# Performance work log

Measured on AMD Instinct MI355X. Metric: run time of the kernel, lower is better.

Reference implementation:

```python
import jax, jax.numpy as jnp
import numpy as np

D_MODEL = 1024
N_EXPERTS = 16
D_FF = 4 * D_MODEL
B, T = 2, 2048


def setup_inputs() -> dict:
    key = jax.random.key(0)
    ks = jax.random.split(key, 6)
    s1 = 1.0 / np.sqrt(D_MODEL)
    s2 = 1.0 / np.sqrt(D_FF)
    return {
        "x": jax.random.normal(ks[0], (B, T, D_MODEL), dtype=jnp.float32),
        "W1": jax.random.normal(ks[1], (N_EXPERTS, D_MODEL, D_FF), dtype=jnp.float32) * s1,
        "b1": jnp.zeros((N_EXPERTS, D_FF), dtype=jnp.float32),
        "W2": jax.random.normal(ks[2], (N_EXPERTS, D_FF, D_MODEL), dtype=jnp.float32) * s2,
        "b2": jnp.zeros((N_EXPERTS, D_MODEL), dtype=jnp.float32),
        "Wg": jax.random.normal(ks[3], (D_MODEL, N_EXPERTS), dtype=jnp.float32) * s1,
        "k": 2,
    }


def reference(x, W1, b1, W2, b2, Wg, k):
    # Gating: [B,T,E] logits, top-k, softmax over selected logits
    gate_logits = jnp.einsum("btd,de->bte", x, Wg)
    topk_vals, topk_idx = jax.lax.top_k(gate_logits, k)      # [B,T,k]
    weights = jax.nn.softmax(topk_vals, axis=-1)             # [B,T,k]
    # Dense all-expert FFN (faithful to the original which computes every expert)
    h = jax.nn.swish(jnp.einsum("btd,edf->btef", x, W1) + b1)        # [B,T,E,4D]
    expert_out = jnp.einsum("btef,efd->bted", h, W2) + b2            # [B,T,E,D]
    # Gather top-k expert outputs per token and combine
    sel = jnp.take_along_axis(expert_out, topk_idx[..., None], axis=2)  # [B,T,k,D]
    return jnp.sum(sel * weights[..., None], axis=2)                    # [B,T,D]
```

## Files before the change

### kernel.cpp

```cpp
#include <hip/hip_runtime.h>
#include <cstdint>

#define D_MODEL 1024
#define N_EXP   16
#define D_FF    4096
#define NTOK    4096
#define NSEL    8192

typedef uint16_t u16;
typedef __bf16    bf16x8 __attribute__((ext_vector_type(8)));
typedef uint16_t  u16x8  __attribute__((ext_vector_type(8)));
typedef float     f32x4  __attribute__((ext_vector_type(4)));
typedef uint32_t  u32x2  __attribute__((ext_vector_type(2)));

__device__ __forceinline__ u16 f2bf(float x) {
    union { float f; uint32_t i; } c; c.f = x;
    uint32_t i = c.i + 0x7fffu + ((c.i >> 16) & 1u);
    return (u16)(i >> 16);
}

__device__ __forceinline__ uint32_t cvtpk(float lo, float hi) {
    uint32_t r;
    asm("v_cvt_pk_bf16_f32 %0, %1, %2" : "=v"(r) : "v"(lo), "v"(hi));
    return r;
}

#define ASYNC16(gp, lp) __builtin_amdgcn_global_load_lds( \
    (__attribute__((address_space(1))) void*)(gp),        \
    (__attribute__((address_space(3))) void*)(lp), 16, 0, 0)

__global__ void gate_kernel(const float* __restrict__ x, const float* __restrict__ Wg,
                            int* __restrict__ tok_idx, float* __restrict__ tok_w,
                            int* __restrict__ counts)
{
    const int lane = threadIdx.x & 63;
    const int t = blockIdx.x * 4 + (threadIdx.x >> 6);
    const float* xr = x + (size_t)t * D_MODEL;
    float acc[N_EXP];
    #pragma unroll
    for (int e = 0; e < N_EXP; e++) acc[e] = 0.f;
    for (int d = lane; d < D_MODEL; d += 64) {
        float xv = xr[d];
        const float* wr = Wg + d * N_EXP;
        #pragma unroll
        for (int e = 0; e < N_EXP; e++) acc[e] += xv * wr[e];
    }
    #pragma unroll
    for (int e = 0; e < N_EXP; e++) {
        float v = acc[e];
        #pragma unroll
        for (int o = 32; o > 0; o >>= 1) v += __shfl_xor(v, o, 64);
        acc[e] = v;
    }
    if (lane == 0) {
        int i0 = 0; float v0 = acc[0];
        #pragma unroll
        for (int e = 1; e < N_EXP; e++) if (acc[e] > v0) { v0 = acc[e]; i0 = e; }
        int i1 = (i0 == 0) ? 1 : 0; float v1 = -3.0e38f;
        #pragma unroll
        for (int e = 0; e < N_EXP; e++) if (e != i0 && acc[e] > v1) { v1 = acc[e]; i1 = e; }
        float e1  = __expf(v1 - v0);
        float inv = 1.f / (1.f + e1);
        tok_idx[2 * t] = i0;  tok_idx[2 * t + 1] = i1;
        tok_w[2 * t] = inv;   tok_w[2 * t + 1] = e1 * inv;
        atomicAdd(&counts[i0], 1);
        atomicAdd(&counts[i1], 1);
    }
}

__global__ void scan_kernel(const int* __restrict__ counts, int* __restrict__ offsets,
                            int* __restrict__ cursors)
{
    if (threadIdx.x == 0) {
        int s = 0;
        #pragma unroll
        for (int e = 0; e < N_EXP; e++) { offsets[e] = s; cursors[e] = s; s += counts[e]; }
        offsets[N_EXP] = s;
    }
}

__global__ void scatter_kernel(const int* __restrict__ tok_idx, const float* __restrict__ tok_w,
                               int* __restrict__ cursors, int* __restrict__ perm_token,
                               float* __restrict__ perm_w, int* __restrict__ slots)
{
    const int t = blockIdx.x * 256 + threadIdx.x;
    #pragma unroll
    for (int j = 0; j < 2; j++) {
        int e = tok_idx[2 * t + j];
        int slot = atomicAdd(&cursors[e], 1);
        perm_token[slot] = t;
        perm_w[slot] = tok_w[2 * t + j];
        slots[2 * t + j] = slot;
    }
}

__global__ void gatherA_kernel(const float* __restrict__ x, const int* __restrict__ perm_token,
                               u16* __restrict__ Abf)
{
    const int slot = blockIdx.x;
    const int t = perm_token[slot];
    const float* src = x + (size_t)t * D_MODEL;
    u16* dst = Abf + (size_t)slot * D_MODEL;
    const int d = threadIdx.x * 4;
    f32x4 v = *(const f32x4*)(src + d);
    u32x2 o;
    o.x = cvtpk(v[0], v[1]);
    o.y = cvtpk(v[2], v[3]);
    *(u32x2*)(dst + d) = o;
}

template<bool SWISH>
__global__ __launch_bounds__(256, 3)
void gemm_kernel(const u16* __restrict__ A, const float* __restrict__ W,
                 const float* __restrict__ bias, const int* __restrict__ offsets,
                 const float* __restrict__ perm_w,
                 u16* __restrict__ Hout, float* __restrict__ Yout,
                 int K, int N)
{
    const int e   = blockIdx.z;
    const int off = offsets[e];
    const int cnt = offsets[e + 1] - off;
    const int m0  = blockIdx.y * 128;
    if (m0 >= cnt) return;
    const int n0  = blockIdx.x * 128;

    __shared__ u16 Alds[128 * 32];
    __shared__ u16 Blds[128 * 32];

    const int tid  = threadIdx.x;
    const int lane = tid & 63;
    const int w    = tid >> 6;
    const int wm   = w & 1;
    const int wn   = w >> 1;

    const int arow = w * 16 + (lane >> 2);
    const int oA   = (lane & 3) ^ ((arow >> 1) & 3) ^ ((arow >> 3) & 3);
    int rA = m0 + arow;      if (rA > cnt - 1) rA = cnt - 1;
    int rB = m0 + arow + 64; if (rB > cnt - 1) rB = cnt - 1;
    const u16* aph0 = A + (size_t)(off + rA) * K + oA * 8;
    const u16* aph1 = A + (size_t)(off + rB) * K + oA * 8;

    const int fo = tid & 15;
    const int dp = tid >> 4;
    const int k0 = 2 * dp;
    const float* bbase = W + (size_t)e * K * N + n0 + fo * 8;
    const int koct = dp >> 2;
    const int kin  = k0 & 7;
    uint32_t* bwp[8];
    #pragma unroll
    for (int j = 0; j < 8; j++) {
        const int row = fo * 8 + j;
        const int oct = koct ^ (fo & 3) ^ ((j >> 1) & 3);
        bwp[j] = (uint32_t*)&Blds[row * 32 + oct * 8 + kin];
    }

    const int q = lane >> 4;
    int a_rd[4];
    #pragma unroll
    for (int mi = 0; mi < 4; mi++) {
        const int r   = wm * 64 + mi * 16 + (lane & 15);
        const int oct = q ^ ((r >> 1) & 3) ^ ((r >> 3) & 3);
        a_rd[mi] = r * 32 + oct * 8;
    }
    const int fbase = wn * 64 + (lane & 15);
    int b_rd[4];
    #pragma unroll
    for (int ni = 0; ni < 4; ni++) {
        const int f   = fbase + ni * 16;
        const int oct = q ^ ((f >> 1) & 3) ^ ((f >> 3) & 3);
        b_rd[ni] = f * 32 + oct * 8;
    }

    f32x4 acc[4][4] = {};

    for (int kt = 0; kt < K; kt += 32) {
        ASYNC16(aph0 + kt, &Alds[w * 512]);
        ASYNC16(aph1 + kt, &Alds[(w + 4) * 512]);
        {
            const float* bp = bbase + (size_t)kt * N;
            f32x4 w00 = *(const f32x4*)(bp + (size_t)k0 * N);
            f32x4 w01 = *(const f32x4*)(bp + (size_t)k0 * N + 4);
            f32x4 w10 = *(const f32x4*)(bp + (size_t)(k0 + 1) * N);
            f32x4 w11 = *(const f32x4*)(bp + (size_t)(k0 + 1) * N + 4);
            #pragma unroll
            for (int j = 0; j < 4; j++) *bwp[j]     = cvtpk(w00[j], w10[j]);
            #pragma unroll
            for (int j = 0; j < 4; j++) *bwp[4 + j] = cvtpk(w01[j], w11[j]);
        }
        __syncthreads();

        u16x8 af[4], bfr[4];
        #pragma unroll
        for (int mi = 0; mi < 4; mi++) af[mi] = *(const u16x8*)(&Alds[a_rd[mi]]);
        #pragma unroll
        for (int ni = 0; ni < 4; ni++) bfr[ni] = *(const u16x8*)(&Blds[b_rd[ni]]);
        #pragma unroll
        for (int mi = 0; mi < 4; mi++)
            #pragma unroll
            for (int ni = 0; ni < 4; ni++)
                acc[mi][ni] = __builtin_amdgcn_mfma_f32_16x16x32_bf16(
                    __builtin_bit_cast(bf16x8, af[mi]),
                    __builtin_bit_cast(bf16x8, bfr[ni]),
                    acc[mi][ni], 0, 0, 0);
        __syncthreads();
    }

    const int rowq = (lane >> 4) * 4;
    #pragma unroll
    for (int mi = 0; mi < 4; mi++) {
        #pragma unroll
        for (int r = 0; r < 4; r++) {
            const int m = m0 + wm * 64 + mi * 16 + rowq + r;
            if (m < cnt) {
                const size_t gm = (size_t)(off + m);
                float pw = SWISH ? 0.f : perm_w[gm];
                #pragma unroll
                for (int ni = 0; ni < 4; ni++) {
                    const int gn = n0 + fbase + ni * 16;
                    float c = acc[mi][ni][r] + bias[(size_t)e * N + gn];
                    if (SWISH) {
                        float s = c / (1.f + __expf(-c));
                        Hout[gm * (size_t)N + gn] = f2bf(s);
                    } else {
                        Yout[gm * (size_t)N + gn] = c * pw;
                    }
                }
            }
        }
    }
}

__global__ void combine_kernel(const float* __restrict__ Y, const int* __restrict__ slots,
                               float* __restrict__ out)
{
    const int idx = blockIdx.x * 256 + threadIdx.x;
    const int t = idx >> 8;
    const int d = (idx & 255) * 4;
    const int s0 = slots[2 * t], s1 = slots[2 * t + 1];
    f32x4 a = *(const f32x4*)(Y + (size_t)s0 * D_MODEL + d);
    f32x4 b = *(const f32x4*)(Y + (size_t)s1 * D_MODEL + d);
    f32x4 o = a + b;
    *(f32x4*)(out + (size_t)t * D_MODEL + d) = o;
}

extern "C" void kernel_launch(void* const* d_in, const int* in_sizes, int n_in,
                              void* d_out, int out_size, void* d_ws, size_t ws_size,
                              hipStream_t stream)
{
    const float* x  = (const float*)d_in[0];
    const float* W1 = (const float*)d_in[1];
    const float* b1 = (const float*)d_in[2];
    const float* W2 = (const float*)d_in[3];
    const float* b2 = (const float*)d_in[4];
    const float* Wg = (const float*)d_in[5];

    char* ws = (char*)d_ws;
    int*   counts     = (int*)(ws);
    int*   offsets    = (int*)(ws + 64);
    int*   cursors    = (int*)(ws + 192);
    int*   tok_idx    = (int*)(ws + 256);
    float* tok_w      = (float*)(ws + 256 + 32768);
    int*   slots      = (int*)(ws + 256 + 2 * 32768);
    int*   perm_token = (int*)(ws + 256 + 3 * 32768);
    float* perm_w     = (float*)(ws + 256 + 4 * 32768);
    u16*   h          = (u16*)(ws + 262144);
    float* Yslot      = (float*)(ws + 262144 + (size_t)NSEL * D_FF * 2);
    u16*   Abf        = (u16*)Yslot;

    hipMemsetAsync(counts, 0, 64, stream);
    gate_kernel<<<dim3(NTOK / 4), dim3(256), 0, stream>>>(x, Wg, tok_idx, tok_w, counts);
    scan_kernel<<<dim3(1), dim3(64), 0, stream>>>(counts, offsets, cursors);
    scatter_kernel<<<dim3(NTOK / 256), dim3(256), 0, stream>>>(tok_idx, tok_w, cursors,
                                                               perm_token, perm_w, slots);
    gatherA_kernel<<<dim3(NSEL), dim3(256), 0, stream>>>(x, perm_token, Abf);
    gemm_kernel<true><<<dim3(32, 32, 16), dim3(256), 0, stream>>>(
        Abf, W1, b1, offsets, nullptr, h, nullptr, D_MODEL, D_FF);
    gemm_kernel<false><<<dim3(8, 32, 16), dim3(256), 0, stream>>>(
        (const u16*)h, W2, b2, offsets, perm_w, nullptr, Yslot, D_FF, D_MODEL);
    combine_kernel<<<dim3(NTOK), dim3(256), 0, stream>>>(Yslot, slots, (float*)d_out);
}
```

Before: 970.2 us.

## Double-buffer GEMM LDS tiles, split-K the second GEMM with atomic combine

Both expert GEMMs now double-buffer their A and B shared-memory tiles. The next tile's global loads are issued before the current tile's MFMAs, which cuts one barrier per k-step and hides load latency. The down-projection GEMM is split four ways along K to raise block count, and it atomically accumulates weighted results straight into the zeroed output. This removes the Yslot buffer and the combine kernel, at the cost of double the LDS per block, fp32 atomic contention, and nondeterministic summation order.

```diff
diff --git a/kernel.cpp b/kernel.cpp
--- a/kernel.cpp
+++ b/kernel.cpp
@@ -81,7 +81,7 @@
 
 __global__ void scatter_kernel(const int* __restrict__ tok_idx, const float* __restrict__ tok_w,
                                int* __restrict__ cursors, int* __restrict__ perm_token,
-                               float* __restrict__ perm_w, int* __restrict__ slots)
+                               float* __restrict__ perm_w)
 {
     const int t = blockIdx.x * 256 + threadIdx.x;
     #pragma unroll
@@ -90,7 +90,6 @@
         int slot = atomicAdd(&cursors[e], 1);
         perm_token[slot] = t;
         perm_w[slot] = tok_w[2 * t + j];
-        slots[2 * t + j] = slot;
     }
 }
 
@@ -109,23 +108,27 @@
     *(u32x2*)(dst + d) = o;
 }
 
-template<bool SWISH>
+template<bool SWISH, int KSPLIT>
 __global__ __launch_bounds__(256, 3)
 void gemm_kernel(const u16* __restrict__ A, const float* __restrict__ W,
                  const float* __restrict__ bias, const int* __restrict__ offsets,
-                 const float* __restrict__ perm_w,
+                 const int* __restrict__ perm_token, const float* __restrict__ perm_w,
                  u16* __restrict__ Hout, float* __restrict__ Yout,
                  int K, int N)
 {
-    const int e   = blockIdx.z;
+    const int zz  = blockIdx.z;
+    const int e   = zz & (N_EXP - 1);
+    const int ks  = zz >> 4;
     const int off = offsets[e];
     const int cnt = offsets[e + 1] - off;
     const int m0  = blockIdx.y * 128;
     if (m0 >= cnt) return;
     const int n0  = blockIdx.x * 128;
-
-    __shared__ u16 Alds[128 * 32];
-    __shared__ u16 Blds[128 * 32];
+    const int kbase  = ks * (K / KSPLIT);
+    const int ksteps = (K / KSPLIT) / 32;
+
+    __shared__ u16 Alds[2][128 * 32];
+    __shared__ u16 Blds[2][128 * 32];
 
     const int tid  = threadIdx.x;
     const int lane = tid & 63;
@@ -146,12 +149,12 @@
     const float* bbase = W + (size_t)e * K * N + n0 + fo * 8;
     const int koct = dp >> 2;
     const int kin  = k0 & 7;
-    uint32_t* bwp[8];
+    int boff[8];
     #pragma unroll
     for (int j = 0; j < 8; j++) {
         const int row = fo * 8 + j;
         const int oct = koct ^ (fo & 3) ^ ((j >> 1) & 3);
-        bwp[j] = (uint32_t*)&Blds[row * 32 + oct * 8 + kin];
+        boff[j] = row * 32 + oct * 8 + kin;
     }
 
     const int q = lane >> 4;
@@ -173,27 +176,41 @@
 
     f32x4 acc[4][4] = {};
 
-    for (int kt = 0; kt < K; kt += 32) {
-        ASYNC16(aph0 + kt, &Alds[w * 512]);
-        ASYNC16(aph1 + kt, &Alds[(w + 4) * 512]);
-        {
-            const float* bp = bbase + (size_t)kt * N;
-            f32x4 w00 = *(const f32x4*)(bp + (size_t)k0 * N);
-            f32x4 w01 = *(const f32x4*)(bp + (size_t)k0 * N + 4);
-            f32x4 w10 = *(const f32x4*)(bp + (size_t)(k0 + 1) * N);
-            f32x4 w11 = *(const f32x4*)(bp + (size_t)(k0 + 1) * N + 4);
-            #pragma unroll
-            for (int j = 0; j < 4; j++) *bwp[j]     = cvtpk(w00[j], w10[j]);
-            #pragma unroll
-            for (int j = 0; j < 4; j++) *bwp[4 + j] = cvtpk(w01[j], w11[j]);
+    {
+        ASYNC16(aph0 + kbase, &Alds[0][w * 512]);
+        ASYNC16(aph1 + kbase, &Alds[0][(w + 4) * 512]);
+        const float* bp = bbase + (size_t)kbase * N;
+        f32x4 w00 = *(const f32x4*)(bp + (size_t)k0 * N);
+        f32x4 w01 = *(const f32x4*)(bp + (size_t)k0 * N + 4);
+        f32x4 w10 = *(const f32x4*)(bp + (size_t)(k0 + 1) * N);
+        f32x4 w11 = *(const f32x4*)(bp + (size_t)(k0 + 1) * N + 4);
+        #pragma unroll
+        for (int j = 0; j < 4; j++) *(uint32_t*)&Blds[0][boff[j]]     = cvtpk(w00[j], w10[j]);
+        #pragma unroll
+        for (int j = 0; j < 4; j++) *(uint32_t*)&Blds[0][boff[4 + j]] = cvtpk(w01[j], w11[j]);
+    }
+    __syncthreads();
+
+    int cur = 0;
+    for (int i = 0; i < ksteps; ++i) {
+        const bool has_next = (i + 1 < ksteps);
+        f32x4 w00, w01, w10, w11;
+        if (has_next) {
+            const int ktn = kbase + (i + 1) * 32;
+            ASYNC16(aph0 + ktn, &Alds[cur ^ 1][w * 512]);
+            ASYNC16(aph1 + ktn, &Alds[cur ^ 1][(w + 4) * 512]);
+            const float* bp = bbase + (size_t)ktn * N;
+            w00 = *(const f32x4*)(bp + (size_t)k0 * N);
+            w01 = *(const f32x4*)(bp + (size_t)k0 * N + 4);
+            w10 = *(const f32x4*)(bp + (size_t)(k0 + 1) * N);
+            w11 = *(const f32x4*)(bp + (size_t)(k0 + 1) * N + 4);
         }
-        __syncthreads();
 
         u16x8 af[4], bfr[4];
         #pragma unroll
-        for (int mi = 0; mi < 4; mi++) af[mi] = *(const u16x8*)(&Alds[a_rd[mi]]);
-        #pragma unroll
-        for (int ni = 0; ni < 4; ni++) bfr[ni] = *(const u16x8*)(&Blds[b_rd[ni]]);
+        for (int mi = 0; mi < 4; mi++) af[mi] = *(const u16x8*)(&Alds[cur][a_rd[mi]]);
+        #pragma unroll
+        for (int ni = 0; ni < 4; ni++) bfr[ni] = *(const u16x8*)(&Blds[cur][b_rd[ni]]);
         #pragma unroll
         for (int mi = 0; mi < 4; mi++)
             #pragma unroll
@@ -202,7 +219,15 @@
                     __builtin_bit_cast(bf16x8, af[mi]),
                     __builtin_bit_cast(bf16x8, bfr[ni]),
                     acc[mi][ni], 0, 0, 0);
-        __syncthreads();
+
+        if (has_next) {
+            #pragma unroll
+            for (int j = 0; j < 4; j++) *(uint32_t*)&Blds[cur ^ 1][boff[j]]     = cvtpk(w00[j], w10[j]);
+            #pragma unroll
+            for (int j = 0; j < 4; j++) *(uint32_t*)&Blds[cur ^ 1][boff[4 + j]] = cvtpk(w01[j], w11[j]);
+            __syncthreads();
+            cur ^= 1;
+        }
     }
 
     const int rowq = (lane >> 4) * 4;
@@ -213,34 +238,29 @@
             const int m = m0 + wm * 64 + mi * 16 + rowq + r;
             if (m < cnt) {
                 const size_t gm = (size_t)(off + m);
-                float pw = SWISH ? 0.f : perm_w[gm];
-                #pragma unroll
-                for (int ni = 0; ni < 4; ni++) {
-                    const int gn = n0 + fbase + ni * 16;
-                    float c = acc[mi][ni][r] + bias[(size_t)e * N + gn];
-                    if (SWISH) {
+                if constexpr (SWISH) {
+                    #pragma unroll
+                    for (int ni = 0; ni < 4; ni++) {
+                        const int gn = n0 + fbase + ni * 16;
+                        float c = acc[mi][ni][r] + bias[(size_t)e * N + gn];
                         float s = c / (1.f + __expf(-c));
                         Hout[gm * (size_t)N + gn] = f2bf(s);
-                    } else {
-                        Yout[gm * (size_t)N + gn] = c * pw;
+                    }
+                } else {
+                    const int   tok = perm_token[gm];
+                    const float pw  = perm_w[gm];
+                    float* orow = Yout + (size_t)tok * N;
+                    #pragma unroll
+                    for (int ni = 0; ni < 4; ni++) {
+                        const int gn = n0 + fbase + ni * 16;
+                        float c = acc[mi][ni][r];
+                        if (ks == 0) c += bias[(size_t)e * N + gn];
+                        atomicAdd(&orow[gn], c * pw);
                     }
                 }
             }
         }
     }
-}
-
-__global__ void combine_kernel(const float* __restrict__ Y, const int* __restrict__ slots,
-                               float* __restrict__ out)
-{
-    const int idx = blockIdx.x * 256 + threadIdx.x;
-    const int t = idx >> 8;
-    const int d = (idx & 255) * 4;
-    const int s0 = slots[2 * t], s1 = slots[2 * t + 1];
-    f32x4 a = *(const f32x4*)(Y + (size_t)s0 * D_MODEL + d);
-    f32x4 b = *(const f32x4*)(Y + (size_t)s1 * D_MODEL + d);
-    f32x4 o = a + b;
-    *(f32x4*)(out + (size_t)t * D_MODEL + d) = o;
 }
 
 extern "C" void kernel_launch(void* const* d_in, const int* in_sizes, int n_in,
@@ -260,22 +280,20 @@
     int*   cursors    = (int*)(ws + 192);
     int*   tok_idx    = (int*)(ws + 256);
     float* tok_w      = (float*)(ws + 256 + 32768);
-    int*   slots      = (int*)(ws + 256 + 2 * 32768);
-    int*   perm_token = (int*)(ws + 256 + 3 * 32768);
-    float* perm_w     = (float*)(ws + 256 + 4 * 32768);
+    int*   perm_token = (int*)(ws + 256 + 2 * 32768);
+    float* perm_w     = (float*)(ws + 256 + 3 * 32768);
     u16*   h          = (u16*)(ws + 262144);
-    float* Yslot      = (float*)(ws + 262144 + (size_t)NSEL * D_FF * 2);
-    u16*   Abf        = (u16*)Yslot;
+    u16*   Abf        = (u16*)(ws + 262144 + (size_t)NSEL * D_FF * 2);
 
     hipMemsetAsync(counts, 0, 64, stream);
+    hipMemsetAsync(d_out, 0, out_size, stream);
     gate_kernel<<<dim3(NTOK / 4), dim3(256), 0, stream>>>(x, Wg, tok_idx, tok_w, counts);
     scan_kernel<<<dim3(1), dim3(64), 0, stream>>>(counts, offsets, cursors);
     scatter_kernel<<<dim3(NTOK / 256), dim3(256), 0, stream>>>(tok_idx, tok_w, cursors,
-                                                               perm_token, perm_w, slots);
+                                                               perm_token, perm_w);
     gatherA_kernel<<<dim3(NSEL), dim3(256), 0, stream>>>(x, perm_token, Abf);
-    gemm_kernel<true><<<dim3(32, 32, 16), dim3(256), 0, stream>>>(
-        Abf, W1, b1, offsets, nullptr, h, nullptr, D_MODEL, D_FF);
-    gemm_kernel<false><<<dim3(8, 32, 16), dim3(256), 0, stream>>>(
-        (const u16*)h, W2, b2, offsets, perm_w, nullptr, Yslot, D_FF, D_MODEL);
-    combine_kernel<<<dim3(NTOK), dim3(256), 0, stream>>>(Yslot, slots, (float*)d_out);
-}
+    gemm_kernel<true, 1><<<dim3(32, 32, 16), dim3(256), 0, stream>>>(
+        Abf, W1, b1, offsets, nullptr, nullptr, h, nullptr, D_MODEL, D_FF);
+    gemm_kernel<false, 4><<<dim3(8, 32, 16 * 4), dim3(256), 0, stream>>>(
+        h, W2, b2, offsets, perm_token, perm_w, nullptr, (float*)d_out, D_FF, D_MODEL);
+}
```

Result: faster. 942.5 us (-2.9%).
